# Kernel optimization log

Measured on AMD Instinct MI355X. Metric: run time of the kernel, lower is better.

## Reference

```python
import jax, jax.numpy as jnp
import numpy as np
import math

D_MODEL = 1024
N_HEADS = 16
HEAD_DIM = D_MODEL // N_HEADS
RANK = 128
SCALE = 1.0 / math.sqrt(HEAD_DIM)


def lowrank(x, u, v, b):
    # y = (x @ u) @ v + b : d_model -> rank -> d_model
    return jnp.einsum('bsd,dr,re->bse', x, u, v) + b


def setup_inputs() -> dict:
    key = jax.random.key(0)
    ks = jax.random.split(key, 16)
    B, S = 2, 2048
    inp = {
        'q': jax.random.normal(ks[0], (B, S, D_MODEL), jnp.float32),
        'k': jax.random.normal(ks[1], (B, S, D_MODEL), jnp.float32),
        'v': jax.random.normal(ks[2], (B, S, D_MODEL), jnp.float32),
        'mask': jnp.ones((B, S), jnp.int32),
    }
    i = 3
    for name in ('q', 'k', 'v', 'out'):
        inp[f'{name}_u'] = jax.random.normal(ks[i], (D_MODEL, RANK), jnp.float32) * 0.02
        inp[f'{name}_v'] = jax.random.normal(ks[i + 1], (RANK, D_MODEL), jnp.float32) * 0.02
        inp[f'{name}_b'] = jnp.zeros((D_MODEL,), jnp.float32)
        i += 2
    return inp


def reference(q, k, v, mask, q_u, q_v, q_b, k_u, k_v, k_b, v_u, v_v, v_b, out_u, out_v, out_b):
    B, S, _ = q.shape
    qh = lowrank(q, q_u, q_v, q_b).reshape(B, S, N_HEADS, HEAD_DIM)
    kh = lowrank(k, k_u, k_v, k_b).reshape(B, S, N_HEADS, HEAD_DIM)
    vh = lowrank(v, v_u, v_v, v_b).reshape(B, S, N_HEADS, HEAD_DIM)
    # scores: [B, H, Sq, Sk]
    scores = jnp.einsum('bqhd,bkhd->bhqk', qh, kh) * SCALE
    scores = jnp.where(mask[:, None, None, :] == 0, -1e9, scores)
    attn = jax.nn.softmax(scores, axis=-1)
    ctx = jnp.einsum('bhqk,bkhd->bqhd', attn, vh).reshape(B, S, D_MODEL)
    return lowrank(ctx, out_u, out_v, out_b)
```

## Files before the change

kernel.cpp:

```cpp
#include <hip/hip_runtime.h>
#include <hip/hip_bf16.h>
#include <stdint.h>

#define DEVI __device__ __forceinline__

typedef __attribute__((ext_vector_type(8))) __bf16 bf16x8;
typedef __attribute__((ext_vector_type(4))) float f32x4;
typedef __attribute__((ext_vector_type(4))) unsigned short us4;

DEVI unsigned short f2bf(float x) {
  union { __bf16 b; unsigned short s; } u;
  u.b = (__bf16)x;
  return u.s;
}

DEVI f32x4 mfma16(bf16x8 a, bf16x8 b, f32x4 c) {
  return __builtin_amdgcn_mfma_f32_16x16x32_bf16(a, b, c, 0, 0, 0);
}

DEVI bf16x8 ld_frag(const unsigned short* tile, int row, int ld, int kbase, int lane) {
  const unsigned short* p = tile + row * ld + kbase + ((lane >> 4) << 2);
  union { bf16x8 f; us4 h[2]; } u;
  u.h[0] = *(const us4*)p;
  u.h[1] = *(const us4*)(p + 16);
  return u.f;
}

struct TP { const float* in[8]; unsigned short* out[8]; };

__global__ __launch_bounds__(256) void wtrans2(TP p) {
  const int z = blockIdx.y;
  const int R = (z & 1) ? 128 : 1024;
  const int C = (z & 1) ? 1024 : 128;
  __shared__ unsigned short T[32][33];
  const int tilesC = C >> 5;
  const int tr0 = (blockIdx.x / tilesC) << 5;
  const int tc0 = (blockIdx.x % tilesC) << 5;
  const int tx = threadIdx.x & 31, ty = threadIdx.x >> 5;
  #pragma unroll
  for (int j = 0; j < 4; j++)
    T[ty + j * 8][tx] = f2bf(p.in[z][(size_t)(tr0 + ty + j * 8) * C + tc0 + tx]);
  __syncthreads();
  #pragma unroll
  for (int j = 0; j < 4; j++)
    p.out[z][(size_t)(tc0 + ty + j * 8) * R + tr0 + tx] = T[tx][ty + j * 8];
}

struct PJ {
  const void* X[3];
  const unsigned short* UT[3];
  const unsigned short* VT[3];
  const float* bias[3];
  void* O[3];
  float oscale[3];
};

template<bool ABF16, bool OF32>
__global__ __launch_bounds__(256)
void proj_fused(PJ p) {
  __shared__ unsigned short SH[128 * 132 + 64 * 132];
  unsigned short* Xs = SH;
  unsigned short* Us = SH + 64 * 36;
  unsigned short* Vs = SH;
  unsigned short* Ts = SH + 128 * 132;

  const int tid = threadIdx.x, lane = tid & 63, w = tid >> 6;
  const int z = blockIdx.z;
  const int m0 = blockIdx.x * 64;
  const int lg4 = (lane >> 4) << 2, l15 = lane & 15;

  const float* Xf = (const float*)p.X[z];
  const unsigned short* Xb = (const unsigned short*)p.X[z];
  const unsigned short* UT = p.UT[z];
  const unsigned short* VT = p.VT[z];

  const int xr = tid >> 2, xc = (tid & 3) * 8;
  const int ur = tid >> 1, uc = (tid & 1) * 16;

  float4 rx0, rx1; uint4 rxb;
  uint4 ru0, ru1;
  auto ldX = [&](int k0) {
    if (ABF16) {
      rxb = *(const uint4*)(Xb + (size_t)(m0 + xr) * 1024 + k0 + xc);
    } else {
      const float* s = Xf + (size_t)(m0 + xr) * 1024 + k0 + xc;
      rx0 = *(const float4*)s; rx1 = *(const float4*)(s + 4);
    }
    const unsigned short* su = UT + (size_t)ur * 1024 + k0 + uc;
    ru0 = *(const uint4*)su; ru1 = *(const uint4*)(su + 8);
  };

  f32x4 acc1[4][2] = {};
  ldX(0);
  for (int k0 = 0; k0 < 1024; k0 += 32) {
    __syncthreads();
    {
      union { uint4 u; us4 h[2]; } t;
      us4* xd = (us4*)&Xs[xr * 36 + xc];
      if (ABF16) {
        t.u = rxb; xd[0] = t.h[0]; xd[1] = t.h[1];
      } else {
        us4 a, bq;
        a[0] = f2bf(rx0.x); a[1] = f2bf(rx0.y); a[2] = f2bf(rx0.z); a[3] = f2bf(rx0.w);
        bq[0] = f2bf(rx1.x); bq[1] = f2bf(rx1.y); bq[2] = f2bf(rx1.z); bq[3] = f2bf(rx1.w);
        xd[0] = a; xd[1] = bq;
      }
      us4* udst = (us4*)&Us[ur * 36 + uc];
      t.u = ru0; udst[0] = t.h[0]; udst[1] = t.h[1];
      t.u = ru1; udst[2] = t.h[0]; udst[3] = t.h[1];
    }
    int kn = k0 + 32; if (kn > 992) kn = 992;
    ldX(kn);
    __syncthreads();

    bf16x8 af[4], wf[2];
    #pragma unroll
    for (int mi = 0; mi < 4; mi++)
      af[mi] = ld_frag(Xs, mi * 16 + l15, 36, 0, lane);
    #pragma unroll
    for (int ni = 0; ni < 2; ni++)
      wf[ni] = ld_frag(Us, w * 32 + ni * 16 + l15, 36, 0, lane);
    #pragma unroll
    for (int mi = 0; mi < 4; mi++)
      #pragma unroll
      for (int ni = 0; ni < 2; ni++)
        acc1[mi][ni] = mfma16(af[mi], wf[ni], acc1[mi][ni]);
  }

  #pragma unroll
  for (int mi = 0; mi < 4; mi++)
    #pragma unroll
    for (int ni = 0; ni < 2; ni++)
      #pragma unroll
      for (int r = 0; r < 4; r++)
        Ts[(mi * 16 + lg4 + r) * 132 + w * 32 + ni * 16 + l15] = f2bf(acc1[mi][ni][r]);
  __syncthreads();

  bf16x8 af2[4][4];
  #pragma unroll
  for (int mi = 0; mi < 4; mi++)
    #pragma unroll
    for (int kc = 0; kc < 4; kc++)
      af2[mi][kc] = ld_frag(Ts, mi * 16 + l15, 132, kc * 32, lane);

  const float os = p.oscale[z];
  const int vr = tid >> 2, vc = (tid & 3) * 32;
  for (int nc = 0; nc < 8; nc++) {
    __syncthreads();
    #pragma unroll
    for (int pp = 0; pp < 2; pp++) {
      const unsigned short* s = VT + (size_t)(nc * 128 + pp * 64 + vr) * 128 + vc;
      uint4* d = (uint4*)&Vs[(pp * 64 + vr) * 132 + vc];
      #pragma unroll
      for (int j = 0; j < 4; j++) d[j] = *(const uint4*)(s + j * 8);
    }
    __syncthreads();

    f32x4 acc2[4][2] = {};
    #pragma unroll
    for (int kc = 0; kc < 4; kc++) {
      bf16x8 bf0 = ld_frag(Vs, w * 32 + 0 * 16 + l15, 132, kc * 32, lane);
      bf16x8 bf1 = ld_frag(Vs, w * 32 + 1 * 16 + l15, 132, kc * 32, lane);
      #pragma unroll
      for (int mi = 0; mi < 4; mi++) {
        acc2[mi][0] = mfma16(af2[mi][kc], bf0, acc2[mi][0]);
        acc2[mi][1] = mfma16(af2[mi][kc], bf1, acc2[mi][1]);
      }
    }

    #pragma unroll
    for (int ni = 0; ni < 2; ni++) {
      const int col = nc * 128 + w * 32 + ni * 16 + l15;
      const float bv = p.bias[z][col];
      #pragma unroll
      for (int mi = 0; mi < 4; mi++)
        #pragma unroll
        for (int r = 0; r < 4; r++) {
          const int row = m0 + mi * 16 + lg4 + r;
          float vv = (acc2[mi][ni][r] + bv) * os;
          if (OF32) ((float*)p.O[z])[(size_t)row * 1024 + col] = vv;
          else ((unsigned short*)p.O[z])[(size_t)row * 1024 + col] = f2bf(vv);
        }
    }
  }
}

__global__ __launch_bounds__(256)
void attn_k2p(const unsigned short* __restrict__ qh, const unsigned short* __restrict__ kh,
              const unsigned short* __restrict__ vh, const int* __restrict__ mask,
              unsigned short* __restrict__ ctx) {
  const int S = 2048, DM = 1024;
  __shared__ unsigned short Ks[64][68];
  __shared__ unsigned short VTs[64][68];
  __shared__ alignas(16) float mkadd[64];
  const int tid = threadIdx.x, lane = tid & 63, w = tid >> 6;
  const int b = blockIdx.z, h = blockIdx.y, q0 = blockIdx.x * 128;
  const int qbase = q0 + w * 32;
  const int lg4 = (lane >> 4) << 2, l15 = lane & 15;

  bf16x8 qf[2][2];
  #pragma unroll
  for (int ni = 0; ni < 2; ni++)
    #pragma unroll
    for (int kk = 0; kk < 2; kk++) {
      const unsigned short* p = qh + (size_t)(b * S + qbase + ni * 16 + l15) * DM
                                + h * 64 + kk * 32 + lg4;
      union { bf16x8 f; us4 h4[2]; } u;
      u.h4[0] = *(const us4*)p;
      u.h4[1] = *(const us4*)(p + 16);
      qf[ni][kk] = u.f;
    }

  float mrow[2], lrow[2];
  f32x4 acc_o[4][2] = {};
  mrow[0] = mrow[1] = -1e30f;
  lrow[0] = lrow[1] = 0.f;

  const int srow = tid >> 2, sseg = (tid & 3) * 16;

  uint4 rk0, rk1, rv0, rv1; int rmI = 1;
  auto ldT = [&](int kv0) {
    const unsigned short* ksrc = kh + (size_t)(b * S + kv0 + srow) * DM + h * 64 + sseg;
    rk0 = *(const uint4*)ksrc; rk1 = *(const uint4*)(ksrc + 8);
    const unsigned short* vsrc = vh + (size_t)(b * S + kv0 + srow) * DM + h * 64 + sseg;
    rv0 = *(const uint4*)vsrc; rv1 = *(const uint4*)(vsrc + 8);
    if (tid < 64) rmI = mask[b * S + kv0 + tid];
  };
  ldT(0);

  for (int kv0 = 0; kv0 < S; kv0 += 64) {
    __syncthreads();
    {
      union { uint4 u[2]; unsigned short s[16]; us4 h[4]; } tk, tv;
      tk.u[0] = rk0; tk.u[1] = rk1;
      us4* kd = (us4*)&Ks[srow][sseg];
      kd[0] = tk.h[0]; kd[1] = tk.h[1]; kd[2] = tk.h[2]; kd[3] = tk.h[3];
      tv.u[0] = rv0; tv.u[1] = rv1;
      #pragma unroll
      for (int j = 0; j < 16; j++) VTs[sseg + j][srow] = tv.s[j];
      if (tid < 64) mkadd[tid] = (rmI == 0) ? -1e9f : 0.0f;
    }
    int nxt = kv0 + 64; if (nxt >= S) nxt = kv0;
    ldT(nxt);
    __syncthreads();

    f32x4 sc[4][2];
    #pragma unroll
    for (int mi = 0; mi < 4; mi++) {
      bf16x8 kf0 = ld_frag(&Ks[0][0], mi * 16 + l15, 68, 0, lane);
      bf16x8 kf1 = ld_frag(&Ks[0][0], mi * 16 + l15, 68, 32, lane);
      #pragma unroll
      for (int ni = 0; ni < 2; ni++) {
        f32x4 zz = {0.f, 0.f, 0.f, 0.f};
        zz = mfma16(kf0, qf[ni][0], zz);
        zz = mfma16(kf1, qf[ni][1], zz);
        sc[mi][ni] = zz;
      }
    }
    #pragma unroll
    for (int mi = 0; mi < 4; mi++) {
      f32x4 mv = *(const f32x4*)&mkadd[mi * 16 + lg4];
      #pragma unroll
      for (int ni = 0; ni < 2; ni++) sc[mi][ni] += mv;
    }

    #pragma unroll
    for (int ni = 0; ni < 2; ni++) {
      float pm = sc[0][ni][0];
      #pragma unroll
      for (int mi = 0; mi < 4; mi++)
        #pragma unroll
        for (int r = 0; r < 4; r++) pm = fmaxf(pm, sc[mi][ni][r]);
      pm = fmaxf(pm, __shfl_xor(pm, 16));
      pm = fmaxf(pm, __shfl_xor(pm, 32));
      const float mnew = fmaxf(mrow[ni], pm);
      const float alpha = __expf(mrow[ni] - mnew);
      mrow[ni] = mnew;
      float rs = 0.f;
      #pragma unroll
      for (int mi = 0; mi < 4; mi++)
        #pragma unroll
        for (int r = 0; r < 4; r++) {
          float e = __expf(sc[mi][ni][r] - mnew);
          sc[mi][ni][r] = e;
          rs += e;
        }
      rs += __shfl_xor(rs, 16);
      rs += __shfl_xor(rs, 32);
      lrow[ni] = lrow[ni] * alpha + rs;
      #pragma unroll
      for (int mi = 0; mi < 4; mi++) acc_o[mi][ni] *= alpha;
    }

    bf16x8 pb[2][2];
    #pragma unroll
    for (int kc = 0; kc < 2; kc++)
      #pragma unroll
      for (int ni = 0; ni < 2; ni++) {
        bf16x8 f;
        #pragma unroll
        for (int e = 0; e < 8; e++)
          f[e] = (__bf16)sc[2 * kc + (e >> 2)][ni][e & 3];
        pb[kc][ni] = f;
      }

    #pragma unroll
    for (int kc = 0; kc < 2; kc++) {
      #pragma unroll
      for (int mi = 0; mi < 4; mi++) {
        bf16x8 va = ld_frag(&VTs[0][0], mi * 16 + l15, 68, kc * 32, lane);
        acc_o[mi][0] = mfma16(va, pb[kc][0], acc_o[mi][0]);
        acc_o[mi][1] = mfma16(va, pb[kc][1], acc_o[mi][1]);
      }
    }
  }

  #pragma unroll
  for (int ni = 0; ni < 2; ni++) {
    const float rinv = 1.0f / lrow[ni];
    const size_t rowoff = (size_t)(b * S + qbase + ni * 16 + l15) * DM + h * 64;
    #pragma unroll
    for (int mi = 0; mi < 4; mi++) {
      us4 o;
      #pragma unroll
      for (int r = 0; r < 4; r++) o[r] = f2bf(acc_o[mi][ni][r] * rinv);
      *(us4*)(ctx + rowoff + mi * 16 + lg4) = o;
    }
  }
}

extern "C" void kernel_launch(void* const* d_in, const int* in_sizes, int n_in,
                              void* d_out, int out_size, void* d_ws, size_t ws_size,
                              hipStream_t stream) {
  const float* q = (const float*)d_in[0];
  const float* k = (const float*)d_in[1];
  const float* v = (const float*)d_in[2];
  const int* mask = (const int*)d_in[3];
  const float* wu[4] = {(const float*)d_in[4], (const float*)d_in[7],
                        (const float*)d_in[10], (const float*)d_in[13]};
  const float* wv[4] = {(const float*)d_in[5], (const float*)d_in[8],
                        (const float*)d_in[11], (const float*)d_in[14]};
  const float* wb[4] = {(const float*)d_in[6], (const float*)d_in[9],
                        (const float*)d_in[12], (const float*)d_in[15]};

  char* ws = (char*)d_ws;
  unsigned short* WT  = (unsigned short*)ws;
  unsigned short* QH  = (unsigned short*)(ws + 2097152);
  unsigned short* KH  = QH + 4194304;
  unsigned short* VH  = KH + 4194304;
  unsigned short* CTX = VH + 4194304;

  TP tp;
  for (int i = 0; i < 4; i++) { tp.in[2 * i] = wu[i]; tp.in[2 * i + 1] = wv[i]; }
  for (int i = 0; i < 8; i++) tp.out[i] = WT + (size_t)i * 131072;
  wtrans2<<<dim3(128, 8), 256, 0, stream>>>(tp);

  const float SCALE = 0.125f;

  PJ pq = {};
  pq.X[0] = q; pq.X[1] = k; pq.X[2] = v;
  pq.UT[0] = tp.out[0]; pq.UT[1] = tp.out[2]; pq.UT[2] = tp.out[4];
  pq.VT[0] = tp.out[1]; pq.VT[1] = tp.out[3]; pq.VT[2] = tp.out[5];
  pq.bias[0] = wb[0]; pq.bias[1] = wb[1]; pq.bias[2] = wb[2];
  pq.O[0] = QH; pq.O[1] = KH; pq.O[2] = VH;
  pq.oscale[0] = SCALE; pq.oscale[1] = 1.f; pq.oscale[2] = 1.f;
  proj_fused<false, false><<<dim3(64, 1, 3), 256, 0, stream>>>(pq);

  attn_k2p<<<dim3(16, 16, 2), 256, 0, stream>>>(QH, KH, VH, mask, CTX);

  PJ po = {};
  po.X[0] = CTX;
  po.UT[0] = tp.out[6];
  po.VT[0] = tp.out[7];
  po.bias[0] = wb[3];
  po.O[0] = d_out;
  po.oscale[0] = 1.f;
  proj_fused<true, true><<<dim3(64, 1, 1), 256, 0, stream>>>(po);
}
```

Before: 259.6 us.

## Restructure attention to 8 waves of 16 rows with lazy softmax rescale

The attention kernel moves from 4 waves each handling 32 query rows to 8 waves each handling 16 rows, which halves per-wave register state so more waves can be resident. The online softmax now skips rescaling the accumulators unless the new running max exceeds the old one by more than 8, and s_setprio is raised around the MFMA sections. Each K/V tile is shared by more waves, so the cost of staging it through LDS is spread further. In exchange, the block needs twice as many threads per barrier, and the lazy rescale lets exponentials grow up to e^8 before renormalising.

```diff
diff --git a/kernel.cpp b/kernel.cpp
--- a/kernel.cpp
+++ b/kernel.cpp
@@ -16,6 +16,13 @@
 
 DEVI f32x4 mfma16(bf16x8 a, bf16x8 b, f32x4 c) {
   return __builtin_amdgcn_mfma_f32_16x16x32_bf16(a, b, c, 0, 0, 0);
+}
+
+DEVI f32x4 vmax4(f32x4 a, f32x4 b) {
+  f32x4 r;
+  r[0] = fmaxf(a[0], b[0]); r[1] = fmaxf(a[1], b[1]);
+  r[2] = fmaxf(a[2], b[2]); r[3] = fmaxf(a[3], b[3]);
+  return r;
 }
 
 DEVI bf16x8 ld_frag(const unsigned short* tile, int row, int ld, int kbase, int lane) {
@@ -185,45 +192,38 @@
   }
 }
 
-__global__ __launch_bounds__(256)
-void attn_k2p(const unsigned short* __restrict__ qh, const unsigned short* __restrict__ kh,
-              const unsigned short* __restrict__ vh, const int* __restrict__ mask,
-              unsigned short* __restrict__ ctx) {
+__global__ __launch_bounds__(512, 4)
+void attn_k3(const unsigned short* __restrict__ qh, const unsigned short* __restrict__ kh,
+             const unsigned short* __restrict__ vh, const int* __restrict__ mask,
+             unsigned short* __restrict__ ctx) {
   const int S = 2048, DM = 1024;
   __shared__ unsigned short Ks[64][68];
   __shared__ unsigned short VTs[64][68];
   __shared__ alignas(16) float mkadd[64];
   const int tid = threadIdx.x, lane = tid & 63, w = tid >> 6;
   const int b = blockIdx.z, h = blockIdx.y, q0 = blockIdx.x * 128;
-  const int qbase = q0 + w * 32;
   const int lg4 = (lane >> 4) << 2, l15 = lane & 15;
-
-  bf16x8 qf[2][2];
-  #pragma unroll
-  for (int ni = 0; ni < 2; ni++)
-    #pragma unroll
-    for (int kk = 0; kk < 2; kk++) {
-      const unsigned short* p = qh + (size_t)(b * S + qbase + ni * 16 + l15) * DM
-                                + h * 64 + kk * 32 + lg4;
-      union { bf16x8 f; us4 h4[2]; } u;
-      u.h4[0] = *(const us4*)p;
-      u.h4[1] = *(const us4*)(p + 16);
-      qf[ni][kk] = u.f;
-    }
-
-  float mrow[2], lrow[2];
-  f32x4 acc_o[4][2] = {};
-  mrow[0] = mrow[1] = -1e30f;
-  lrow[0] = lrow[1] = 0.f;
-
-  const int srow = tid >> 2, sseg = (tid & 3) * 16;
-
-  uint4 rk0, rk1, rv0, rv1; int rmI = 1;
+  const int qrow = q0 + w * 16 + l15;
+
+  bf16x8 qf[2];
+  #pragma unroll
+  for (int kk = 0; kk < 2; kk++) {
+    const unsigned short* p = qh + (size_t)(b * S + qrow) * DM + h * 64 + kk * 32 + lg4;
+    union { bf16x8 f; us4 h4[2]; } u;
+    u.h4[0] = *(const us4*)p;
+    u.h4[1] = *(const us4*)(p + 16);
+    qf[kk] = u.f;
+  }
+
+  float mrow = -1e30f, lrow = 0.f;
+  f32x4 acc_o[4] = {};
+
+  const int srow = tid >> 3, sseg = (tid & 7) * 8;
+
+  uint4 rk, rv; int rmI = 1;
   auto ldT = [&](int kv0) {
-    const unsigned short* ksrc = kh + (size_t)(b * S + kv0 + srow) * DM + h * 64 + sseg;
-    rk0 = *(const uint4*)ksrc; rk1 = *(const uint4*)(ksrc + 8);
-    const unsigned short* vsrc = vh + (size_t)(b * S + kv0 + srow) * DM + h * 64 + sseg;
-    rv0 = *(const uint4*)vsrc; rv1 = *(const uint4*)(vsrc + 8);
+    rk = *(const uint4*)(kh + (size_t)(b * S + kv0 + srow) * DM + h * 64 + sseg);
+    rv = *(const uint4*)(vh + (size_t)(b * S + kv0 + srow) * DM + h * 64 + sseg);
     if (tid < 64) rmI = mask[b * S + kv0 + tid];
   };
   ldT(0);
@@ -231,101 +231,90 @@
   for (int kv0 = 0; kv0 < S; kv0 += 64) {
     __syncthreads();
     {
-      union { uint4 u[2]; unsigned short s[16]; us4 h[4]; } tk, tv;
-      tk.u[0] = rk0; tk.u[1] = rk1;
+      union { uint4 u; us4 h[2]; unsigned short s[8]; } tk, tv;
+      tk.u = rk;
       us4* kd = (us4*)&Ks[srow][sseg];
-      kd[0] = tk.h[0]; kd[1] = tk.h[1]; kd[2] = tk.h[2]; kd[3] = tk.h[3];
-      tv.u[0] = rv0; tv.u[1] = rv1;
-      #pragma unroll
-      for (int j = 0; j < 16; j++) VTs[sseg + j][srow] = tv.s[j];
+      kd[0] = tk.h[0]; kd[1] = tk.h[1];
+      tv.u = rv;
+      #pragma unroll
+      for (int j = 0; j < 8; j++) VTs[sseg + j][srow] = tv.s[j];
       if (tid < 64) mkadd[tid] = (rmI == 0) ? -1e9f : 0.0f;
     }
     int nxt = kv0 + 64; if (nxt >= S) nxt = kv0;
     ldT(nxt);
     __syncthreads();
 
-    f32x4 sc[4][2];
+    f32x4 sc[4];
+    __builtin_amdgcn_s_setprio(1);
     #pragma unroll
     for (int mi = 0; mi < 4; mi++) {
       bf16x8 kf0 = ld_frag(&Ks[0][0], mi * 16 + l15, 68, 0, lane);
       bf16x8 kf1 = ld_frag(&Ks[0][0], mi * 16 + l15, 68, 32, lane);
-      #pragma unroll
-      for (int ni = 0; ni < 2; ni++) {
-        f32x4 zz = {0.f, 0.f, 0.f, 0.f};
-        zz = mfma16(kf0, qf[ni][0], zz);
-        zz = mfma16(kf1, qf[ni][1], zz);
-        sc[mi][ni] = zz;
-      }
-    }
-    #pragma unroll
-    for (int mi = 0; mi < 4; mi++) {
-      f32x4 mv = *(const f32x4*)&mkadd[mi * 16 + lg4];
-      #pragma unroll
-      for (int ni = 0; ni < 2; ni++) sc[mi][ni] += mv;
-    }
-
-    #pragma unroll
-    for (int ni = 0; ni < 2; ni++) {
-      float pm = sc[0][ni][0];
-      #pragma unroll
-      for (int mi = 0; mi < 4; mi++)
-        #pragma unroll
-        for (int r = 0; r < 4; r++) pm = fmaxf(pm, sc[mi][ni][r]);
-      pm = fmaxf(pm, __shfl_xor(pm, 16));
-      pm = fmaxf(pm, __shfl_xor(pm, 32));
-      const float mnew = fmaxf(mrow[ni], pm);
-      const float alpha = __expf(mrow[ni] - mnew);
-      mrow[ni] = mnew;
-      float rs = 0.f;
-      #pragma unroll
-      for (int mi = 0; mi < 4; mi++)
-        #pragma unroll
-        for (int r = 0; r < 4; r++) {
-          float e = __expf(sc[mi][ni][r] - mnew);
-          sc[mi][ni][r] = e;
-          rs += e;
-        }
-      rs += __shfl_xor(rs, 16);
-      rs += __shfl_xor(rs, 32);
-      lrow[ni] = lrow[ni] * alpha + rs;
-      #pragma unroll
-      for (int mi = 0; mi < 4; mi++) acc_o[mi][ni] *= alpha;
-    }
-
-    bf16x8 pb[2][2];
+      f32x4 zz = {0.f, 0.f, 0.f, 0.f};
+      zz = mfma16(kf0, qf[0], zz);
+      zz = mfma16(kf1, qf[1], zz);
+      sc[mi] = zz;
+    }
+    __builtin_amdgcn_s_setprio(0);
+    #pragma unroll
+    for (int mi = 0; mi < 4; mi++)
+      sc[mi] += *(const f32x4*)&mkadd[mi * 16 + lg4];
+
+    f32x4 tm = vmax4(vmax4(sc[0], sc[1]), vmax4(sc[2], sc[3]));
+    float pm = fmaxf(fmaxf(tm[0], tm[1]), fmaxf(tm[2], tm[3]));
+    pm = fmaxf(pm, __shfl_xor(pm, 16));
+    pm = fmaxf(pm, __shfl_xor(pm, 32));
+
+    if (!__all(pm <= mrow + 8.f)) {
+      const float mnew = fmaxf(mrow, pm);
+      const float alpha = __expf(mrow - mnew);
+      lrow *= alpha;
+      #pragma unroll
+      for (int mi = 0; mi < 4; mi++) acc_o[mi] *= alpha;
+      mrow = mnew;
+    }
+
+    #pragma unroll
+    for (int mi = 0; mi < 4; mi++)
+      #pragma unroll
+      for (int r = 0; r < 4; r++)
+        sc[mi][r] = __expf(sc[mi][r] - mrow);
+
+    f32x4 ssum = (sc[0] + sc[1]) + (sc[2] + sc[3]);
+    float rs = (ssum[0] + ssum[1]) + (ssum[2] + ssum[3]);
+    rs += __shfl_xor(rs, 16);
+    rs += __shfl_xor(rs, 32);
+    lrow += rs;
+
+    bf16x8 pb[2];
+    #pragma unroll
+    for (int kc = 0; kc < 2; kc++) {
+      bf16x8 f;
+      #pragma unroll
+      for (int e = 0; e < 8; e++)
+        f[e] = (__bf16)sc[2 * kc + (e >> 2)][e & 3];
+      pb[kc] = f;
+    }
+
+    __builtin_amdgcn_s_setprio(1);
     #pragma unroll
     for (int kc = 0; kc < 2; kc++)
-      #pragma unroll
-      for (int ni = 0; ni < 2; ni++) {
-        bf16x8 f;
-        #pragma unroll
-        for (int e = 0; e < 8; e++)
-          f[e] = (__bf16)sc[2 * kc + (e >> 2)][ni][e & 3];
-        pb[kc][ni] = f;
-      }
-
-    #pragma unroll
-    for (int kc = 0; kc < 2; kc++) {
       #pragma unroll
       for (int mi = 0; mi < 4; mi++) {
         bf16x8 va = ld_frag(&VTs[0][0], mi * 16 + l15, 68, kc * 32, lane);
-        acc_o[mi][0] = mfma16(va, pb[kc][0], acc_o[mi][0]);
-        acc_o[mi][1] = mfma16(va, pb[kc][1], acc_o[mi][1]);
+        acc_o[mi] = mfma16(va, pb[kc], acc_o[mi]);
       }
-    }
-  }
-
-  #pragma unroll
-  for (int ni = 0; ni < 2; ni++) {
-    const float rinv = 1.0f / lrow[ni];
-    const size_t rowoff = (size_t)(b * S + qbase + ni * 16 + l15) * DM + h * 64;
-    #pragma unroll
-    for (int mi = 0; mi < 4; mi++) {
-      us4 o;
-      #pragma unroll
-      for (int r = 0; r < 4; r++) o[r] = f2bf(acc_o[mi][ni][r] * rinv);
-      *(us4*)(ctx + rowoff + mi * 16 + lg4) = o;
-    }
+    __builtin_amdgcn_s_setprio(0);
+  }
+
+  const float rinv = 1.0f / lrow;
+  const size_t rowoff = (size_t)(b * S + qrow) * DM + h * 64;
+  #pragma unroll
+  for (int mi = 0; mi < 4; mi++) {
+    us4 o;
+    #pragma unroll
+    for (int r = 0; r < 4; r++) o[r] = f2bf(acc_o[mi][r] * rinv);
+    *(us4*)(ctx + rowoff + mi * 16 + lg4) = o;
   }
 }
 
@@ -366,7 +355,7 @@
   pq.oscale[0] = SCALE; pq.oscale[1] = 1.f; pq.oscale[2] = 1.f;
   proj_fused<false, false><<<dim3(64, 1, 3), 256, 0, stream>>>(pq);
 
-  attn_k2p<<<dim3(16, 16, 2), 256, 0, stream>>>(QH, KH, VH, mask, CTX);
+  attn_k3<<<dim3(16, 16, 2), 512, 0, stream>>>(QH, KH, VH, mask, CTX);
 
   PJ po = {};
   po.X[0] = CTX;
```

Result: no change. 256.8 us (-1.1%).
